# Kernel optimization log

Hardware: AMD Instinct MI355X
Metric: run time of the kernel (lower is better)

## Reference

```python
import jax, jax.numpy as jnp
import numpy as np

OBS, ACT = 128, 32
DM, NST, NLAYERS = 1024, 16, 2
DI = 2 * DM                      # expand=2
R = (DM + 15) // 16              # dt_rank = 64
K = 4                            # d_conv


def setup_inputs() -> dict:
    key = jax.random.key(0)
    ks = jax.random.split(key, 12)
    s = lambda k, shape, scale=0.02: jax.random.normal(k, shape, jnp.float32) * scale
    return {
        "y": jax.random.normal(ks[0], (4, 1024, OBS), jnp.float32),
        "W_in_l": s(ks[1], (DM, OBS)),
        "b_in_l": jnp.zeros((DM,), jnp.float32),
        "W_inproj": s(ks[2], (NLAYERS, 2 * DI, DM)),
        "conv_w": s(ks[3], (NLAYERS, DI, 1, K), 0.2),
        "conv_b": jnp.zeros((NLAYERS, DI), jnp.float32),
        "W_xproj": s(ks[4], (NLAYERS, R + 2 * NST, DI)),
        "W_dt": s(ks[5], (NLAYERS, DI, R)),
        "b_dt": s(ks[6], (NLAYERS, DI), 0.1),
        "A_log": jnp.tile(jnp.log(jnp.arange(1, NST + 1, dtype=jnp.float32))[None, None, :], (NLAYERS, DI, 1)),
        "D": jnp.ones((NLAYERS, DI), jnp.float32),
        "W_outproj": s(ks[7], (NLAYERS, DM, DI)),
        "W_out_l": s(ks[8], (ACT, DM)),
        "b_out_l": jnp.zeros((ACT,), jnp.float32),
    }


def _mamba_block(x, W_inproj, conv_w, conv_b, W_xproj, W_dt, b_dt, A_log, D, W_outproj):
    B, L, _ = x.shape
    xz = jnp.einsum('bld,ed->ble', x, W_inproj)           # [B,L,2*DI]
    xc, z = jnp.split(xz, 2, axis=-1)
    # depthwise causal conv over time
    xc_ncl = jnp.moveaxis(xc, 1, 2)                        # [B,DI,L]
    xc_ncl = jax.lax.conv_general_dilated(
        xc_ncl, conv_w, (1,), [(K - 1, 0)],
        dimension_numbers=('NCH', 'OIH', 'NCH'), feature_group_count=DI)
    xc = jax.nn.silu(jnp.moveaxis(xc_ncl, 1, 2) + conv_b)  # [B,L,DI]
    x_dbl = jnp.einsum('bld,rd->blr', xc, W_xproj)         # [B,L,R+2N]
    dt = jax.nn.softplus(jnp.einsum('blr,dr->bld', x_dbl[..., :R], W_dt) + b_dt)
    Bm = x_dbl[..., R:R + NST]                             # [B,L,N]
    Cm = x_dbl[..., R + NST:]                              # [B,L,N]
    A = -jnp.exp(A_log)                                    # [DI,N]

    def step(h, inp):
        dt_t, x_t, B_t, C_t = inp                          # [B,DI],[B,DI],[B,N],[B,N]
        h = jnp.exp(dt_t[:, :, None] * A) * h + (dt_t * x_t)[:, :, None] * B_t[:, None, :]
        return h, jnp.einsum('bdn,bn->bd', h, C_t)

    tfirst = lambda a: jnp.moveaxis(a, 1, 0)
    h0 = jnp.zeros((B, DI, NST), x.dtype)
    _, ys = jax.lax.scan(step, h0, (tfirst(dt), tfirst(xc), tfirst(Bm), tfirst(Cm)))
    y = (jnp.moveaxis(ys, 0, 1) + D * xc) * jax.nn.silu(z)
    return jnp.einsum('bld,od->blo', y, W_outproj)


def reference(y, W_in_l, b_in_l, W_inproj, conv_w, conv_b, W_xproj, W_dt, b_dt,
              A_log, D, W_outproj, W_out_l, b_out_l):
    x = jnp.einsum('blo,do->bld', y, W_in_l) + b_in_l
    for i in range(NLAYERS):
        x = _mamba_block(x, W_inproj[i], conv_w[i], conv_b[i], W_xproj[i],
                         W_dt[i], b_dt[i], A_log[i], D[i], W_outproj[i])
    return jnp.einsum('bld,od->blo', x, W_out_l) + b_out_l
```

## Files before the change

kernel.cpp:

```cpp
#include <hip/hip_runtime.h>
#include <math.h>

#define OBS 128
#define ACTN 32
#define DM 1024
#define NST 16
#define NLAYERS 2
#define DI 2048
#define RR 64
#define KCONV 4
#define BB 4
#define LL 1024
#define ML (BB*LL)
#define NCHUNK 32
#define CLEN (LL/NCHUNK)

typedef unsigned short u16;
typedef __bf16 bf16x8 __attribute__((ext_vector_type(8)));
typedef float f32x4 __attribute__((ext_vector_type(4)));

__device__ __forceinline__ float siluf(float x) {
    return x / (1.f + __expf(-x));
}

__device__ __forceinline__ size_t smap(size_t i) {
    return (i >> 11) * (2 * DI) + (i & (DI - 1));
}

template<int ACTMODE>
__global__ __launch_bounds__(256)
void gemm_nt(const float* __restrict__ A, int lda,
             const float* __restrict__ W,
             const float* __restrict__ bias,
             float* __restrict__ C, int ldc,
             int N, int K)
{
    __shared__ float As[16][68];
    __shared__ float Ws[16][68];
    const int tid = threadIdx.x;
    const int tx = tid & 15, ty = tid >> 4;
    const int bm = blockIdx.x * 64;
    const int bn = blockIdx.y * 64;
    const int kz = blockIdx.z;
    const int Kc = K / gridDim.z;
    const int kbeg = kz * Kc;
    const int lrow = tid >> 2;
    const int lk = (tid & 3) * 4;
    float acc[4][4] = {};

    for (int k0 = kbeg; k0 < kbeg + Kc; k0 += 16) {
        float4 av = *(const float4*)(A + (size_t)(bm + lrow) * lda + k0 + lk);
        float4 wv = make_float4(0.f, 0.f, 0.f, 0.f);
        if (bn + lrow < N)
            wv = *(const float4*)(W + (size_t)(bn + lrow) * K + k0 + lk);
        As[lk+0][lrow] = av.x; As[lk+1][lrow] = av.y;
        As[lk+2][lrow] = av.z; As[lk+3][lrow] = av.w;
        Ws[lk+0][lrow] = wv.x; Ws[lk+1][lrow] = wv.y;
        Ws[lk+2][lrow] = wv.z; Ws[lk+3][lrow] = wv.w;
        __syncthreads();
        #pragma unroll
        for (int k = 0; k < 16; ++k) {
            const float4 a4 = *(const float4*)&As[k][ty * 4];
            const float4 b4 = *(const float4*)&Ws[k][tx * 4];
            const float av_[4] = {a4.x, a4.y, a4.z, a4.w};
            const float bv_[4] = {b4.x, b4.y, b4.z, b4.w};
            #pragma unroll
            for (int i = 0; i < 4; ++i)
                #pragma unroll
                for (int j = 0; j < 4; ++j)
                    acc[i][j] = fmaf(av_[i], bv_[j], acc[i][j]);
        }
        __syncthreads();
    }

    float* Cp = C + (size_t)kz * ML * ldc;
    #pragma unroll
    for (int i = 0; i < 4; ++i) {
        const int row = bm + ty * 4 + i;
        #pragma unroll
        for (int j = 0; j < 4; ++j) {
            const int col = bn + tx * 4 + j;
            if (col < N) {
                float v = acc[i][j];
                if (bias) v += bias[col];
                if (ACTMODE == 1) v = (v > 20.f) ? v : log1pf(__expf(v));
                Cp[(size_t)row * ldc + col] = v;
            }
        }
    }
}

__global__ __launch_bounds__(256)
void reduce_k(const float* __restrict__ P, float* __restrict__ O, int ks, size_t n,
              const float* __restrict__ bias, int ldc)
{
    const size_t i4 = ((size_t)blockIdx.x * 256 + threadIdx.x) * 4;
    float4 s = *(const float4*)(P + i4);
    for (int z = 1; z < ks; ++z) {
        const float4 p = *(const float4*)(P + (size_t)z * n + i4);
        s.x += p.x; s.y += p.y; s.z += p.z; s.w += p.w;
    }
    if (bias) {
        const int c = (int)(i4 % ldc);
        s.x += bias[c]; s.y += bias[c+1]; s.z += bias[c+2]; s.w += bias[c+3];
    }
    *(float4*)(O + i4) = s;
}

__device__ __forceinline__ u16 f2bf(float x) {
    unsigned u = __float_as_uint(x);
    u += 0x7fffu + ((u >> 16) & 1u);
    return (u16)(u >> 16);
}
__device__ __forceinline__ float bf2f(u16 h) {
    return __uint_as_float(((unsigned)h) << 16);
}
__device__ __forceinline__ void split1(float x, u16& h, u16& m) {
    h = f2bf(x); float r = x - bf2f(h);
    m = f2bf(r);
}

__global__ __launch_bounds__(256)
void split2_k(const float* __restrict__ X, int lda, int K, u16* __restrict__ O, int shift)
{
    const size_t i4 = (size_t)blockIdx.x * 256 + threadIdx.x;
    const size_t row = i4 >> shift;
    const int k = (int)(i4 & ((1u << shift) - 1)) << 2;
    const float4 x = *(const float4*)(X + row * (size_t)lda + k);
    ushort4 h, m;
    split1(x.x, h.x, m.x);
    split1(x.y, h.y, m.y);
    split1(x.z, h.z, m.z);
    split1(x.w, h.w, m.w);
    u16* base = O + row * (size_t)(2 * K) + k;
    *(ushort4*)(base)     = h;
    *(ushort4*)(base + K) = m;
}

template<int TN>
__global__ __launch_bounds__(256)
void gemm3(const u16* __restrict__ A3, const u16* __restrict__ B3,
           float* __restrict__ C, int N, int K, int ldc)
{
    constexpr int MI = (TN == 128) ? 4 : 2;
    constexpr int NJ = 4;
    constexpr int AR = 4;
    constexpr int BR = (TN == 128) ? 4 : 2;
    __shared__ u16 As[2][128][32];
    __shared__ u16 Bs[2][TN][32];
    const int tid = threadIdx.x;
    const int bm = blockIdx.x * 128;
    const int bn = blockIdx.y * TN;

    const int wave = tid >> 6;
    const int lane = tid & 63;
    const int wm = (TN == 128) ? ((wave >> 1) << 6) : (wave << 5);
    const int wn = (TN == 128) ? ((wave & 1) << 6) : 0;
    const int lrow = lane & 15;
    const int lsl = lane >> 4;
    const size_t ld2 = 2 * (size_t)K;

    size_t goffA[AR], goffB[BR];
    int ldsbA[AR], ldsbB[BR];
    #pragma unroll
    for (int r = 0; r < AR; ++r) {
        const int e = (r * 256 + tid) * 8;
        const int plane = e >> 12;
        const int row = (e >> 5) & 127;
        const int slot = (e >> 3) & 3;
        const int kk = ((slot ^ ((row >> 1) & 3)) << 3);
        ldsbA[r] = e * 2;
        goffA[r] = (size_t)(bm + row) * ld2 + (size_t)plane * K + kk;
    }
    #pragma unroll
    for (int r = 0; r < BR; ++r) {
        const int e = (r * 256 + tid) * 8;
        const int plane = e / (TN * 32);
        const int row = (e >> 5) & (TN - 1);
        const int slot = (e >> 3) & 3;
        const int kk = ((slot ^ ((row >> 1) & 3)) << 3);
        ldsbB[r] = e * 2;
        goffB[r] = (size_t)(bn + row) * ld2 + (size_t)plane * K + kk;
    }

    f32x4 acc[MI][NJ];
    #pragma unroll
    for (int i = 0; i < MI; ++i)
        #pragma unroll
        for (int j = 0; j < NJ; ++j)
            acc[i][j] = (f32x4){0.f, 0.f, 0.f, 0.f};

    for (int k0 = 0; k0 < K; k0 += 32) {
        __builtin_amdgcn_sched_barrier(0);
        #pragma unroll
        for (int r = 0; r < AR; ++r)
            __builtin_amdgcn_global_load_lds(
                (const __attribute__((address_space(1))) void*)(A3 + goffA[r] + k0),
                (__attribute__((address_space(3))) void*)((char*)&As[0][0][0] + ldsbA[r]),
                16, 0, 0);
        #pragma unroll
        for (int r = 0; r < BR; ++r)
            __builtin_amdgcn_global_load_lds(
                (const __attribute__((address_space(1))) void*)(B3 + goffB[r] + k0),
                (__attribute__((address_space(3))) void*)((char*)&Bs[0][0][0] + ldsbB[r]),
                16, 0, 0);
        __builtin_amdgcn_sched_barrier(0);
        asm volatile("s_waitcnt vmcnt(0)" ::: "memory");
        __syncthreads();

        bf16x8 bf[NJ][2];
        #pragma unroll
        for (int nj = 0; nj < NJ; ++nj) {
            const int brow = wn + nj * 16 + lrow;
            const int bsl = lsl ^ ((brow >> 1) & 3);
            #pragma unroll
            for (int p = 0; p < 2; ++p)
                bf[nj][p] = *(const bf16x8*)&Bs[p][brow][bsl << 3];
        }
        #pragma unroll
        for (int mi = 0; mi < MI; ++mi) {
            const int arow = wm + mi * 16 + lrow;
            const int asl = lsl ^ ((arow >> 1) & 3);
            const bf16x8 a0 = *(const bf16x8*)&As[0][arow][asl << 3];
            const bf16x8 a1 = *(const bf16x8*)&As[1][arow][asl << 3];
            #pragma unroll
            for (int nj = 0; nj < NJ; ++nj) {
                f32x4 c = acc[mi][nj];
                c = __builtin_amdgcn_mfma_f32_16x16x32_bf16(a0, bf[nj][0], c, 0, 0, 0);
                c = __builtin_amdgcn_mfma_f32_16x16x32_bf16(a1, bf[nj][0], c, 0, 0, 0);
                c = __builtin_amdgcn_mfma_f32_16x16x32_bf16(a0, bf[nj][1], c, 0, 0, 0);
                acc[mi][nj] = c;
            }
        }
        __syncthreads();
        __builtin_amdgcn_sched_barrier(0);
    }

    #pragma unroll
    for (int mi = 0; mi < MI; ++mi) {
        #pragma unroll
        for (int nj = 0; nj < NJ; ++nj) {
            const int r0 = bm + wm + mi * 16 + (lsl << 2);
            const int col = bn + wn + nj * 16 + lrow;
            #pragma unroll
            for (int j = 0; j < 4; ++j)
                C[(size_t)(r0 + j) * ldc + col] = acc[mi][nj][j];
        }
    }
}

__global__ __launch_bounds__(256)
void conv_silu_k(const float* __restrict__ xz,
                 const float* __restrict__ cw,
                 const float* __restrict__ cb,
                 float* __restrict__ xc)
{
    const int c = blockIdx.x * 256 + threadIdx.x;
    const int l = blockIdx.y;
    const int b = blockIdx.z;
    const float4 w4 = *(const float4*)(cw + (size_t)c * 4);
    const float wv[4] = {w4.x, w4.y, w4.z, w4.w};
    float acc = cb[c];
    const float* base = xz + (size_t)b * LL * (2 * DI) + c;
    #pragma unroll
    for (int k = 0; k < 4; ++k) {
        const int ls = l - 3 + k;
        if (ls >= 0) acc = fmaf(base[(size_t)ls * (2 * DI)], wv[k], acc);
    }
    xc[((size_t)b * LL + l) * DI + c] = siluf(acc);
}

__global__ __launch_bounds__(256)
void scan_p1(const float* __restrict__ dt,
             const float* __restrict__ xc,
             const float* __restrict__ xdbl,
             const float* __restrict__ A_log,
             float* __restrict__ xz)
{
    __shared__ float Bs[CLEN][NST];
    const int d = blockIdx.x * 256 + threadIdx.x;
    const int c = blockIdx.y;
    const int b = blockIdx.z;
    const int l0 = c * CLEN;

    for (int i = threadIdx.x; i < CLEN * NST; i += 256) {
        const int r = i >> 4, n = i & 15;
        Bs[r][n] = xdbl[((size_t)b * LL + l0 + r) * 96 + RR + n];
    }
    __syncthreads();

    float An[NST], h[NST];
    {
        const float4* ap4 = (const float4*)(A_log + (size_t)d * NST);
        #pragma unroll
        for (int q = 0; q < 4; ++q) {
            const float4 v = ap4[q];
            An[q*4+0] = -__expf(v.x); An[q*4+1] = -__expf(v.y);
            An[q*4+2] = -__expf(v.z); An[q*4+3] = -__expf(v.w);
        }
    }
    #pragma unroll
    for (int n = 0; n < NST; ++n) h[n] = 0.f;

    const float* dtp = dt + ((size_t)b * LL + l0) * DI + d;
    const float* xp  = xc + ((size_t)b * LL + l0) * DI + d;
    float S = 0.f;

    for (int l = 0; l < CLEN; ++l) {
        const float dtv = dtp[(size_t)l * DI];
        const float xv  = xp[(size_t)l * DI];
        const float bx  = dtv * xv;
        S += dtv;
        const float4 B0 = *(const float4*)&Bs[l][0];
        const float4 B1 = *(const float4*)&Bs[l][4];
        const float4 B2 = *(const float4*)&Bs[l][8];
        const float4 B3 = *(const float4*)&Bs[l][12];
        const float Bv[NST] = {B0.x,B0.y,B0.z,B0.w, B1.x,B1.y,B1.z,B1.w,
                               B2.x,B2.y,B2.z,B2.w, B3.x,B3.y,B3.z,B3.w};
        #pragma unroll
        for (int n = 0; n < NST; ++n) {
            const float a = __expf(dtv * An[n]);
            h[n] = fmaf(a, h[n], bx * Bv[n]);
        }
    }

    const size_t idx0 = (((size_t)c * BB + b) * DI + d) * NST;
    float ap[NST];
    #pragma unroll
    for (int n = 0; n < NST; ++n) ap[n] = __expf(S * An[n]);
    #pragma unroll
    for (int q = 0; q < 4; ++q) {
        *(float4*)&xz[smap(idx0 + q * 4)] = make_float4(ap[q*4],ap[q*4+1],ap[q*4+2],ap[q*4+3]);
        *(float4*)&xz[smap(idx0 + q * 4 + (size_t)ML * DI / 2)] = make_float4(h[q*4],h[q*4+1],h[q*4+2],h[q*4+3]);
    }
}

__global__ __launch_bounds__(256)
void scan_p2(float* __restrict__ xz)
{
    const int t = threadIdx.x;
    const int b = blockIdx.x >> 7;
    const int dgrp = blockIdx.x & 127;
    const int n = t & 15;
    const int d = (dgrp << 4) + (t >> 4);
    float h = 0.f;
    for (int c = 0; c < NCHUNK; ++c) {
        const size_t idx = (((size_t)c * BB + b) * DI + d) * NST + n;
        const size_t ia = smap(idx);
        const size_t ih = smap(idx + (size_t)ML * DI / 2);
        const float ap = xz[ia];
        const float he = xz[ih];
        xz[ih] = h;
        h = fmaf(ap, h, he);
    }
}

__global__ __launch_bounds__(256)
void scan_p3(float* __restrict__ dt_ys,
             const float* __restrict__ xc,
             const float* __restrict__ xdbl,
             const float* __restrict__ A_log,
             const float* __restrict__ xz,
             const float* __restrict__ Dv)
{
    __shared__ float BCs[CLEN][2 * NST];
    const int d = blockIdx.x * 256 + threadIdx.x;
    const int c = blockIdx.y;
    const int b = blockIdx.z;
    const int l0 = c * CLEN;

    for (int i = threadIdx.x; i < CLEN * 2 * NST; i += 256) {
        const int r = i >> 5, n = i & 31;
        BCs[r][n] = xdbl[((size_t)b * LL + l0 + r) * 96 + RR + n];
    }
    __syncthreads();

    float An[NST], h[NST];
    {
        const float4* ap4 = (const float4*)(A_log + (size_t)d * NST);
        #pragma unroll
        for (int q = 0; q < 4; ++q) {
            const float4 v = ap4[q];
            An[q*4+0] = -__expf(v.x); An[q*4+1] = -__expf(v.y);
            An[q*4+2] = -__expf(v.z); An[q*4+3] = -__expf(v.w);
        }
    }
    const size_t idx0 = (((size_t)c * BB + b) * DI + d) * NST;
    #pragma unroll
    for (int q = 0; q < 4; ++q) {
        const float4 v = *(const float4*)&xz[smap(idx0 + q * 4 + (size_t)ML * DI / 2)];
        h[q*4+0] = v.x; h[q*4+1] = v.y; h[q*4+2] = v.z; h[q*4+3] = v.w;
    }
    const float Dd = Dv[d];

    float* dtp = dt_ys + ((size_t)b * LL + l0) * DI + d;
    const float* xp = xc + ((size_t)b * LL + l0) * DI + d;
    const float* zp = xz + ((size_t)b * LL + l0) * (2 * DI) + DI + d;

    for (int l = 0; l < CLEN; ++l) {
        const float dtv = dtp[(size_t)l * DI];
        const float xv  = xp[(size_t)l * DI];
        const float zv  = zp[(size_t)l * (2 * DI)];
        const float bx  = dtv * xv;
        const float4 B0 = *(const float4*)&BCs[l][0];
        const float4 B1 = *(const float4*)&BCs[l][4];
        const float4 B2 = *(const float4*)&BCs[l][8];
        const float4 B3 = *(const float4*)&BCs[l][12];
        const float4 C0 = *(const float4*)&BCs[l][16];
        const float4 C1 = *(const float4*)&BCs[l][20];
        const float4 C2 = *(const float4*)&BCs[l][24];
        const float4 C3 = *(const float4*)&BCs[l][28];
        const float Bv[NST] = {B0.x,B0.y,B0.z,B0.w, B1.x,B1.y,B1.z,B1.w,
                               B2.x,B2.y,B2.z,B2.w, B3.x,B3.y,B3.z,B3.w};
        const float Cv[NST] = {C0.x,C0.y,C0.z,C0.w, C1.x,C1.y,C1.z,C1.w,
                               C2.x,C2.y,C2.z,C2.w, C3.x,C3.y,C3.z,C3.w};
        float y0 = 0.f, y1 = 0.f, y2 = 0.f, y3 = 0.f;
        #pragma unroll
        for (int q = 0; q < 4; ++q) {
            const float a0 = __expf(dtv * An[q*4+0]);
            const float a1 = __expf(dtv * An[q*4+1]);
            const float a2 = __expf(dtv * An[q*4+2]);
            const float a3 = __expf(dtv * An[q*4+3]);
            h[q*4+0] = fmaf(a0, h[q*4+0], bx * Bv[q*4+0]);
            h[q*4+1] = fmaf(a1, h[q*4+1], bx * Bv[q*4+1]);
            h[q*4+2] = fmaf(a2, h[q*4+2], bx * Bv[q*4+2]);
            h[q*4+3] = fmaf(a3, h[q*4+3], bx * Bv[q*4+3]);
            y0 = fmaf(h[q*4+0], Cv[q*4+0], y0);
            y1 = fmaf(h[q*4+1], Cv[q*4+1], y1);
            y2 = fmaf(h[q*4+2], Cv[q*4+2], y2);
            y3 = fmaf(h[q*4+3], Cv[q*4+3], y3);
        }
        const float yv = (y0 + y1) + (y2 + y3);
        dtp[(size_t)l * DI] = fmaf(Dd, xv, yv) * siluf(zv);
    }
}

extern "C" void kernel_launch(void* const* d_in, const int* in_sizes, int n_in,
                              void* d_out, int out_size, void* d_ws, size_t ws_size,
                              hipStream_t stream)
{
    const float* y        = (const float*)d_in[0];
    const float* W_in_l   = (const float*)d_in[1];
    const float* b_in_l   = (const float*)d_in[2];
    const float* W_inproj = (const float*)d_in[3];
    const float* conv_w   = (const float*)d_in[4];
    const float* conv_b   = (const float*)d_in[5];
    const float* W_xproj  = (const float*)d_in[6];
    const float* W_dt     = (const float*)d_in[7];
    const float* b_dt     = (const float*)d_in[8];
    const float* A_log    = (const float*)d_in[9];
    const float* Dvec     = (const float*)d_in[10];
    const float* W_outprj = (const float*)d_in[11];
    const float* W_out_l  = (const float*)d_in[12];
    const float* b_out_l  = (const float*)d_in[13];
    float* out = (float*)d_out;

    float* X    = (float*)d_ws;
    float* XZ   = X    + (size_t)ML * DM;
    float* XC   = XZ   + (size_t)ML * 2 * DI;
    float* XDBL = XC   + (size_t)ML * DI;
    float* DTb  = XDBL + (size_t)ML * 96;
    u16* SCR = (u16*)XC;

    dim3 blk(256);

    gemm_nt<0><<<dim3(ML/64, DM/64, 1), blk, 0, stream>>>(y, OBS, W_in_l, b_in_l, X, DM, DM, OBS);

    for (int layer = 0; layer < NLAYERS; ++layer) {
        const float* Wip = W_inproj + (size_t)layer * 2 * DI * DM;
        const float* cw  = conv_w   + (size_t)layer * DI * KCONV;
        const float* cb  = conv_b   + (size_t)layer * DI;
        const float* Wxp = W_xproj  + (size_t)layer * (RR + 2 * NST) * DI;
        const float* Wdt = W_dt     + (size_t)layer * DI * RR;
        const float* bdt = b_dt     + (size_t)layer * DI;
        const float* Al  = A_log    + (size_t)layer * DI * NST;
        const float* Dl  = Dvec     + (size_t)layer * DI;
        const float* Wop = W_outprj + (size_t)layer * DM * DI;

        u16* A3i = SCR;
        u16* W3i = SCR + (size_t)ML * 2 * DM;
        split2_k<<<dim3((ML * DM / 4) / 256), blk, 0, stream>>>(X, DM, DM, A3i, 8);
        split2_k<<<dim3((2 * DI * DM / 4) / 256), blk, 0, stream>>>(Wip, DM, DM, W3i, 8);
        gemm3<128><<<dim3(ML/128, (2*DI)/128), blk, 0, stream>>>(A3i, W3i, XZ, 2*DI, DM, 2*DI);

        conv_silu_k<<<dim3(DI/256, LL, BB), blk, 0, stream>>>(XZ, cw, cb, XC);

        gemm_nt<0><<<dim3(ML/64, 2, 8), blk, 0, stream>>>(XC, DI, Wxp, nullptr, DTb, 96, 96, DI);
        reduce_k<<<dim3((ML * 96 / 4) / 256), blk, 0, stream>>>(DTb, XDBL, 8, (size_t)ML * 96, nullptr, 96);

        gemm_nt<1><<<dim3(ML/64, DI/64, 1), blk, 0, stream>>>(XDBL, 96, Wdt, bdt, DTb, DI, DI, RR);

        scan_p1<<<dim3(DI/256, NCHUNK, BB), blk, 0, stream>>>(DTb, XC, XDBL, Al, XZ);
        scan_p2<<<dim3(BB * 128), blk, 0, stream>>>(XZ);
        scan_p3<<<dim3(DI/256, NCHUNK, BB), blk, 0, stream>>>(DTb, XC, XDBL, Al, XZ, Dl);

        u16* A3o = (u16*)XZ;
        u16* W3o = (u16*)XZ + (size_t)ML * 2 * DI;
        split2_k<<<dim3((ML * DI / 4) / 256), blk, 0, stream>>>(DTb, DI, DI, A3o, 9);
        split2_k<<<dim3((DM * DI / 4) / 256), blk, 0, stream>>>(Wop, DI, DI, W3o, 9);
        gemm3<64><<<dim3(ML/128, DM/64), blk, 0, stream>>>(A3o, W3o, X, DM, DI, DM);
    }

    gemm_nt<0><<<dim3(ML/64, 1, 8), blk, 0, stream>>>(X, DM, W_out_l, nullptr, XC, ACTN, ACTN, DM);
    reduce_k<<<dim3((ML * ACTN / 4) / 256), blk, 0, stream>>>(XC, out, 8, (size_t)ML * ACTN, b_out_l, ACTN);
}
```

Measured before the change: 860.2 us.

## Double-buffer gemm3 LDS tiles and slide conv window over 32 timesteps

The bf16-split GEMM now keeps two LDS stages and issues the global-to-LDS loads for the next K-slice before computing on the current one, so load latency overlaps with the MFMA work. This doubles the shared memory per block, which may reduce occupancy. The depthwise causal conv kernel now has each thread walk 32 consecutive timesteps with a sliding register window, so each input is read once instead of four times. That second change also launches fewer blocks, which means less parallelism.

```diff
diff --git a/kernel.cpp b/kernel.cpp
--- a/kernel.cpp
+++ b/kernel.cpp
@@ -146,8 +146,8 @@
     constexpr int NJ = 4;
     constexpr int AR = 4;
     constexpr int BR = (TN == 128) ? 4 : 2;
-    __shared__ u16 As[2][128][32];
-    __shared__ u16 Bs[2][TN][32];
+    __shared__ u16 As[2][2][128][32];
+    __shared__ u16 Bs[2][2][TN][32];
     const int tid = threadIdx.x;
     const int bm = blockIdx.x * 128;
     const int bn = blockIdx.y * TN;
@@ -183,6 +183,21 @@
         goffB[r] = (size_t)(bn + row) * ld2 + (size_t)plane * K + kk;
     }
 
+    auto stage = [&](int buf, int kk) {
+        #pragma unroll
+        for (int r = 0; r < AR; ++r)
+            __builtin_amdgcn_global_load_lds(
+                (const __attribute__((address_space(1))) void*)(A3 + goffA[r] + kk),
+                (__attribute__((address_space(3))) void*)((char*)&As[buf][0][0][0] + ldsbA[r]),
+                16, 0, 0);
+        #pragma unroll
+        for (int r = 0; r < BR; ++r)
+            __builtin_amdgcn_global_load_lds(
+                (const __attribute__((address_space(1))) void*)(B3 + goffB[r] + kk),
+                (__attribute__((address_space(3))) void*)((char*)&Bs[buf][0][0][0] + ldsbB[r]),
+                16, 0, 0);
+    };
+
     f32x4 acc[MI][NJ];
     #pragma unroll
     for (int i = 0; i < MI; ++i)
@@ -190,23 +205,15 @@
         for (int j = 0; j < NJ; ++j)
             acc[i][j] = (f32x4){0.f, 0.f, 0.f, 0.f};
 
+    stage(0, 0);
+    __builtin_amdgcn_sched_barrier(0);
+    asm volatile("s_waitcnt vmcnt(0)" ::: "memory");
+    __syncthreads();
+
+    int cur = 0;
     for (int k0 = 0; k0 < K; k0 += 32) {
+        if (k0 + 32 < K) stage(cur ^ 1, k0 + 32);
         __builtin_amdgcn_sched_barrier(0);
-        #pragma unroll
-        for (int r = 0; r < AR; ++r)
-            __builtin_amdgcn_global_load_lds(
-                (const __attribute__((address_space(1))) void*)(A3 + goffA[r] + k0),
-                (__attribute__((address_space(3))) void*)((char*)&As[0][0][0] + ldsbA[r]),
-                16, 0, 0);
-        #pragma unroll
-        for (int r = 0; r < BR; ++r)
-            __builtin_amdgcn_global_load_lds(
-                (const __attribute__((address_space(1))) void*)(B3 + goffB[r] + k0),
-                (__attribute__((address_space(3))) void*)((char*)&Bs[0][0][0] + ldsbB[r]),
-                16, 0, 0);
-        __builtin_amdgcn_sched_barrier(0);
-        asm volatile("s_waitcnt vmcnt(0)" ::: "memory");
-        __syncthreads();
 
         bf16x8 bf[NJ][2];
         #pragma unroll
@@ -215,14 +222,14 @@
             const int bsl = lsl ^ ((brow >> 1) & 3);
             #pragma unroll
             for (int p = 0; p < 2; ++p)
-                bf[nj][p] = *(const bf16x8*)&Bs[p][brow][bsl << 3];
+                bf[nj][p] = *(const bf16x8*)&Bs[cur][p][brow][bsl << 3];
         }
         #pragma unroll
         for (int mi = 0; mi < MI; ++mi) {
             const int arow = wm + mi * 16 + lrow;
             const int asl = lsl ^ ((arow >> 1) & 3);
-            const bf16x8 a0 = *(const bf16x8*)&As[0][arow][asl << 3];
-            const bf16x8 a1 = *(const bf16x8*)&As[1][arow][asl << 3];
+            const bf16x8 a0 = *(const bf16x8*)&As[cur][0][arow][asl << 3];
+            const bf16x8 a1 = *(const bf16x8*)&As[cur][1][arow][asl << 3];
             #pragma unroll
             for (int nj = 0; nj < NJ; ++nj) {
                 f32x4 c = acc[mi][nj];
@@ -232,8 +239,10 @@
                 acc[mi][nj] = c;
             }
         }
+        __builtin_amdgcn_sched_barrier(0);
+        asm volatile("s_waitcnt vmcnt(0)" ::: "memory");
         __syncthreads();
-        __builtin_amdgcn_sched_barrier(0);
+        cur ^= 1;
     }
 
     #pragma unroll
@@ -256,18 +265,21 @@
                  float* __restrict__ xc)
 {
     const int c = blockIdx.x * 256 + threadIdx.x;
-    const int l = blockIdx.y;
+    const int l0 = blockIdx.y * 32;
     const int b = blockIdx.z;
     const float4 w4 = *(const float4*)(cw + (size_t)c * 4);
-    const float wv[4] = {w4.x, w4.y, w4.z, w4.w};
-    float acc = cb[c];
+    const float bias = cb[c];
     const float* base = xz + (size_t)b * LL * (2 * DI) + c;
-    #pragma unroll
-    for (int k = 0; k < 4; ++k) {
-        const int ls = l - 3 + k;
-        if (ls >= 0) acc = fmaf(base[(size_t)ls * (2 * DI)], wv[k], acc);
-    }
-    xc[((size_t)b * LL + l) * DI + c] = siluf(acc);
+    float x0 = (l0 >= 3) ? base[(size_t)(l0 - 3) * (2 * DI)] : 0.f;
+    float x1 = (l0 >= 2) ? base[(size_t)(l0 - 2) * (2 * DI)] : 0.f;
+    float x2 = (l0 >= 1) ? base[(size_t)(l0 - 1) * (2 * DI)] : 0.f;
+    float* op = xc + ((size_t)b * LL + l0) * DI + c;
+    for (int i = 0; i < 32; ++i) {
+        const float x3 = base[(size_t)(l0 + i) * (2 * DI)];
+        const float acc = fmaf(w4.x, x0, fmaf(w4.y, x1, fmaf(w4.z, x2, fmaf(w4.w, x3, bias))));
+        op[(size_t)i * DI] = siluf(acc);
+        x0 = x1; x1 = x2; x2 = x3;
+    }
 }
 
 __global__ __launch_bounds__(256)
@@ -483,7 +495,7 @@
         split2_k<<<dim3((2 * DI * DM / 4) / 256), blk, 0, stream>>>(Wip, DM, DM, W3i, 8);
         gemm3<128><<<dim3(ML/128, (2*DI)/128), blk, 0, stream>>>(A3i, W3i, XZ, 2*DI, DM, 2*DI);
 
-        conv_silu_k<<<dim3(DI/256, LL, BB), blk, 0, stream>>>(XZ, cw, cb, XC);
+        conv_silu_k<<<dim3(DI/256, LL/32, BB), blk, 0, stream>>>(XZ, cw, cb, XC);
 
         gemm_nt<0><<<dim3(ML/64, 2, 8), blk, 0, stream>>>(XC, DI, Wxp, nullptr, DTb, 96, 96, DI);
         reduce_k<<<dim3((ML * 96 / 4) / 256), blk, 0, stream>>>(DTb, XDBL, 8, (size_t)ML * 96, nullptr, 96);
```

After: 797.2 us. 1.08x faster.
